# Optimization experiments

Measured on AMD Instinct MI355X. Metric: run time of the kernel, lower is better.

## Reference

```python
import jax, jax.numpy as jnp
import numpy as np

N = 256          # num_nodes per graph
B = 64           # batch_size (len(data.y))
NLAY = 3
F_IN = 5
NE = N * N       # num_edges per graph
NN = B * N       # total nodes
TEMP = 0.6
ALPHA = 0.1      # propagation residual alpha
BB_ALPHA = 0.8   # BBEdge_pred alpha
K = 2


def setup_inputs() -> dict:
    key = jax.random.key(0)
    ks = jax.random.split(key, 8)
    n_tril = N * (N + 1) // 2
    x = jax.random.normal(ks[0], (NN, F_IN), jnp.float32)
    # lower-triangular (incl. diagonal) entries of the learned adjacency
    edge_weight_param = jax.random.normal(ks[1], (n_tril,), jnp.float32)
    # BBEdge_pred params per layer (torch init: U(1.0,1.5), U(0.49,0.51))
    a_uc = 1.0 + 0.5 * jax.random.uniform(ks[2], (NLAY,), jnp.float32)
    b_uc = 0.49 + 0.02 * jax.random.uniform(ks[3], (NLAY,), jnp.float32)
    # randomness for Kumaraswamy pi sample and RelaxedBernoulli rsample
    u_pi = jax.random.uniform(ks[4], (NLAY,), jnp.float32)
    u_rb = jax.random.uniform(ks[5], (NLAY, NE), jnp.float32)
    lin_w = jax.random.normal(ks[6], (F_IN, 128), jnp.float32) / np.float32(np.sqrt(F_IN))
    lin_b = jnp.zeros((128,), jnp.float32)
    fc_w = jax.random.normal(ks[7], (128, 3), jnp.float32) / np.float32(np.sqrt(128))
    fc_b = jnp.zeros((3,), jnp.float32)
    # dense block-diagonal edge_index: graph b owns nodes [b*N, (b+1)*N); edge k=i*N+j -> (i,j)
    base = jnp.arange(N, dtype=jnp.int32)
    rows = jnp.repeat(base, N)
    cols = jnp.tile(base, N)
    offs = (jnp.arange(B, dtype=jnp.int32) * N)[:, None]
    edge_index = jnp.stack([(offs + rows[None, :]).reshape(-1),
                            (offs + cols[None, :]).reshape(-1)])
    batch = jnp.repeat(jnp.arange(B, dtype=jnp.int32), N)
    return {"x": x, "edge_weight_param": edge_weight_param, "a_uc": a_uc, "b_uc": b_uc,
            "u_pi": u_pi, "u_rb": u_rb, "lin_w": lin_w, "lin_b": lin_b,
            "fc_w": fc_w, "fc_b": fc_b, "edge_index": edge_index, "batch": batch}


def _forward(x, edge_weight_param, a_uc, b_uc, u_pi, u_rb,
             lin_w, lin_b, fc_w, fc_b, edge_index, batch):
    row, col = edge_index[0], edge_index[1]
    # symmetrized dense edge-weight matrix from tril params
    xs, ys = jnp.tril_indices(N)
    W = jnp.zeros((N, N), x.dtype).at[xs, ys].set(edge_weight_param)
    W = W + W.T - jnp.diag(jnp.diag(W))
    w_full = jnp.tile(W.reshape(-1), B)                      # [E]
    # GCN-style degree normalization (self-loops already on diagonal)
    deg = jax.ops.segment_sum(jnp.abs(w_full), row, num_segments=NN)
    dis = jnp.where(deg > 0, deg ** -0.5, 0.0)
    adj = dis[row] * w_full * dis[col]                       # [E]

    # Beta-Bernoulli edge keep-prob and RelaxedBernoulli masks
    a = jax.nn.softplus(jnp.clip(a_uc, -10.0, None))
    b = jax.nn.softplus(jnp.clip(b_uc, -10.0, 50.0))
    up = jnp.clip(u_pi, 1e-6, 1.0 - 1e-6)
    pi = (1.0 - up ** (1.0 / b)) ** (1.0 / a)                # [NLAY]
    ur = jnp.clip(u_rb, 1e-6, 1.0 - 1e-6)
    logits = jnp.log(pi) - jnp.log1p(-pi)                    # [NLAY]
    z = jax.nn.sigmoid((logits[:, None] + jnp.log(ur) - jnp.log1p(-ur)) / TEMP)  # [NLAY, NE]

    def conv(xx, w_e):
        # emb = alpha*x + (1-alpha)/K * scatter(col, w_e * x[row])
        msg = w_e[:, None] * xx[row]                          # [E, F]
        agg = jax.ops.segment_sum(msg, col, num_segments=NN)
        return ALPHA * xx + (1.0 - ALPHA) / K * agg

    emb = ALPHA * x
    # layer 0: masked adjacency
    x1 = conv(x, jnp.tile(z[0], B) * adj)
    emb = emb + (1.0 - ALPHA) * x1 / NLAY
    # layer 1 (middle): unmasked conv, then masked block conv (nblock=1, fp=5)
    x2 = conv(x1, adj)
    emb = emb + (1.0 - ALPHA) * x2 / NLAY
    x3 = jax.nn.relu(conv(x2[:, :F_IN], jnp.tile(z[1], B) * adj))  # dropout off (eval)
    # layer 2 (last)
    x4 = conv(x3, adj)
    emb = emb + (1.0 - ALPHA) * x4 / NLAY
    o = conv(x4, jnp.tile(z[2], B) * adj)
    out = jax.nn.relu(o @ lin_w + lin_b)                      # [NN, 128]

    # KL regularizer summed over layers
    euler = 0.577215664901532
    kld = ((1.0 - BB_ALPHA / a) * (-euler - jax.scipy.special.digamma(b) - 1.0 / b)
           + jnp.log(a * b + 1e-10) - jnp.log(jnp.float32(BB_ALPHA)) - (b - 1.0) / b)
    kld_loss = jnp.sum(kld)

    pooled = jax.ops.segment_sum(out, batch, num_segments=B)  # global_add_pool -> [B, 128]
    output = pooled @ fc_w + fc_b                             # [B, 3]
    drop_rates = pi[:, None]                                  # [NLAY, 1]
    return output, kld_loss, drop_rates


def reference(x, edge_weight_param, a_uc, b_uc, u_pi, u_rb,
              lin_w, lin_b, fc_w, fc_b, edge_index, batch):
    return _forward(x, edge_weight_param, a_uc, b_uc, u_pi, u_rb,
                    lin_w, lin_b, fc_w, fc_b, edge_index, batch)
```

## Files before the change

kernel.cpp:

```cpp
#include <hip/hip_runtime.h>
#include <math.h>

#define NN_ 256
#define BB_ 64
#define FF_ 5
#define NE_ 65536

#define OFF_SLA 0
#define OFF_SL1 65536
#define OFF_SL3 131072
#define OFF_SL5 196608
#define OFF_DIS 262144

__global__ __launch_bounds__(256) void build_all(
    const float* __restrict__ p, const float* __restrict__ u_rb,
    const float* __restrict__ a_uc, const float* __restrict__ b_uc,
    const float* __restrict__ u_pi, float* __restrict__ ws,
    float* __restrict__ out) {
  const int i = blockIdx.x, j = threadIdx.x;
  const int t = (i >= j) ? (i * (i + 1) / 2 + j) : (j * (j + 1) / 2 + i);
  const float w = p[t];

  __shared__ float sh[NN_];
  __shared__ float slg[3];
  __shared__ float skld[3];
  sh[j] = fabsf(w);

  if (j < 3) {
    const int l = j;
    const float au = fmaxf(a_uc[l], -10.0f);
    const float bu = fminf(fmaxf(b_uc[l], -10.0f), 50.0f);
    const float a = log1pf(expf(au));
    const float b = log1pf(expf(bu));
    const float up = fminf(fmaxf(u_pi[l], 1e-6f), 1.0f - 1e-6f);
    const float pi = powf(1.0f - powf(up, 1.0f / b), 1.0f / a);
    slg[l] = logf(pi) - log1pf(-pi);
    if (i == 0) {
      out[193 + l] = pi;
      float x = b, dg = 0.0f;
      while (x < 6.0f) { dg -= 1.0f / x; x += 1.0f; }
      const float inv = 1.0f / x, inv2 = inv * inv;
      dg += logf(x) - 0.5f * inv
            - inv2 * (1.0f / 12.0f - inv2 * (1.0f / 120.0f - inv2 * (1.0f / 252.0f)));
      const float euler = 0.577215664901532f;
      skld[l] = (1.0f - 0.8f / a) * (-euler - dg - 1.0f / b)
                + logf(a * b + 1e-10f) - logf(0.8f) - (b - 1.0f) / b;
    }
  }
  __syncthreads();

  for (int s = NN_ / 2; s > 0; s >>= 1) {
    if (j < s) sh[j] += sh[j + s];
    __syncthreads();
  }
  if (j == 0) {
    const float deg = sh[0];
    ws[OFF_DIS + i] = (deg > 0.0f) ? (1.0f / sqrtf(deg)) : 0.0f;
    if (i == 0) out[192] = skld[0] + skld[1] + skld[2];
  }

  const float lg0 = slg[0];
  const float lg1 = slg[1];
  const float lg2 = slg[2];
  const int idx = i * NN_ + j;
  const float inv_temp = 1.0f / 0.6f;

  ws[OFF_SLA + idx] = w;

  float u, v;
  u = fminf(fmaxf(u_rb[0 * NE_ + idx], 1e-6f), 1.0f - 1e-6f);
  v = (lg0 + logf(u) - log1pf(-u)) * inv_temp;
  ws[OFF_SL1 + idx] = w / (1.0f + expf(-v));

  u = fminf(fmaxf(u_rb[1 * NE_ + idx], 1e-6f), 1.0f - 1e-6f);
  v = (lg1 + logf(u) - log1pf(-u)) * inv_temp;
  ws[OFF_SL3 + idx] = w / (1.0f + expf(-v));

  u = fminf(fmaxf(u_rb[2 * NE_ + idx], 1e-6f), 1.0f - 1e-6f);
  v = (lg2 + logf(u) - log1pf(-u)) * inv_temp;
  ws[OFF_SL5 + idx] = w / (1.0f + expf(-v));
}

__global__ __launch_bounds__(1024) void batch_chain(
    const float* __restrict__ x0g, const float* __restrict__ ws,
    const float* __restrict__ lin_w, const float* __restrict__ lin_b,
    const float* __restrict__ fc_w, const float* __restrict__ fc_b,
    float* __restrict__ out) {
  const int b = blockIdx.x, tid = threadIdx.x;
  __shared__ float xbuf[2][NN_ * 8];
  __shared__ float sbuf[2][NN_ * 8];
  __shared__ float part[4 * NN_ * 8];
  __shared__ float sdis[NN_];
  float* Xc = xbuf[0];
  float* Xn = xbuf[1];
  float* Sc = sbuf[0];
  float* Sn = sbuf[1];

  for (int ii = tid; ii < NN_; ii += 1024) sdis[ii] = ws[OFF_DIS + ii];
  for (int idx = tid; idx < NN_ * FF_; idx += 1024) {
    const int i = idx / 5, f = idx - 5 * i;
    Xc[i * 8 + f] = x0g[b * (NN_ * FF_) + idx];
  }
  __syncthreads();
  for (int idx = tid; idx < 2048; idx += 1024)
    Sc[idx] = sdis[idx >> 3] * Xc[idx];
  __syncthreads();

  const int q = tid >> 8;
  const int j = tid & 255;
  const int k0 = q * 64;

#pragma unroll
  for (int l = 0; l < 5; ++l) {
    const float* __restrict__ Op =
        ws + (l == 0 ? OFF_SL1 : l == 2 ? OFF_SL3 : l == 4 ? OFF_SL5 : OFF_SLA)
        + j;
    float4 a03 = {0.f, 0.f, 0.f, 0.f};
    float a4 = 0.f;
#pragma unroll 8
    for (int k = k0; k < k0 + 64; ++k) {
      const float wv = Op[k * NN_];
      const float4 xv = *(const float4*)(Sc + k * 8);
      const float x4 = Sc[k * 8 + 4];
      a03.x += wv * xv.x; a03.y += wv * xv.y;
      a03.z += wv * xv.z; a03.w += wv * xv.w;
      a4 += wv * x4;
    }
    *(float4*)(part + tid * 8) = a03;
    part[tid * 8 + 4] = a4;
    __syncthreads();
    for (int idx = tid; idx < 2048; idx += 1024) {
      const float sum = part[idx] + part[2048 + idx] + part[4096 + idx] +
                        part[6144 + idx];
      const float dj = sdis[idx >> 3];
      float y = 0.1f * Xc[idx] + 0.45f * dj * sum;
      if (l == 2) y = fmaxf(y, 0.f);
      Xn[idx] = y;
      Sn[idx] = dj * y;
    }
    __syncthreads();
    float* tp = Xc; Xc = Xn; Xn = tp;
    tp = Sc; Sc = Sn; Sn = tp;
  }

  const int k = tid & 127, seg = tid >> 7;
  const float lw0 = lin_w[0 * 128 + k];
  const float lw1 = lin_w[1 * 128 + k];
  const float lw2 = lin_w[2 * 128 + k];
  const float lw3 = lin_w[3 * 128 + k];
  const float lw4 = lin_w[4 * 128 + k];
  const float lb = lin_b[k];
  float acc = 0.f;
  const int j0 = seg * 32;
#pragma unroll 4
  for (int jj = j0; jj < j0 + 32; ++jj) {
    const float4 ov = *(const float4*)(Xc + jj * 8);
    const float o4 = Xc[jj * 8 + 4];
    const float vv = lb + lw0 * ov.x + lw1 * ov.y + lw2 * ov.z +
                     lw3 * ov.w + lw4 * o4;
    acc += fmaxf(vv, 0.f);
  }
  part[seg * 128 + k] = acc;
  __syncthreads();
  if (tid < 128) {
    float s = 0.f;
#pragma unroll
    for (int s8 = 0; s8 < 8; ++s8) s += part[s8 * 128 + tid];
    part[tid] = s;
  }
  __syncthreads();
  if (tid < 3) {
    float s = fc_b[tid];
    for (int kk = 0; kk < 128; ++kk) s += part[kk] * fc_w[kk * 3 + tid];
    out[b * 3 + tid] = s;
  }
}

extern "C" void kernel_launch(void* const* d_in, const int* in_sizes, int n_in,
                              void* d_out, int out_size, void* d_ws,
                              size_t ws_size, hipStream_t stream) {
  const float* x      = (const float*)d_in[0];
  const float* p      = (const float*)d_in[1];
  const float* a_uc   = (const float*)d_in[2];
  const float* b_uc   = (const float*)d_in[3];
  const float* u_pi   = (const float*)d_in[4];
  const float* u_rb   = (const float*)d_in[5];
  const float* lin_w  = (const float*)d_in[6];
  const float* lin_b  = (const float*)d_in[7];
  const float* fc_w   = (const float*)d_in[8];
  const float* fc_b   = (const float*)d_in[9];
  float* out = (float*)d_out;
  float* ws  = (float*)d_ws;

  build_all<<<256, 256, 0, stream>>>(p, u_rb, a_uc, b_uc, u_pi, ws, out);
  batch_chain<<<64, 1024, 0, stream>>>(x, ws, lin_w, lin_b, fc_w, fc_b, out);
}
```

Measured before the change: 128.0 us.

## Split each graph's propagation chain across four blocks with global-memory barriers

The per-graph chain kernel moves from 64 blocks of 1024 threads to 256 blocks of 256 threads. Each of the four blocks per graph owns a quarter of the output rows. After every layer the blocks exchange the scaled features through global memory and meet at an atomic-counter barrier, and pooling is finished by one block per graph. This fills more compute units on the chip, but it adds inter-block spin-wait synchronisation, which assumes all blocks are co-resident, and extra global traffic.

New measurement: 161.7 us. +26.4%, slower.

```diff
diff --git a/kernel.cpp b/kernel.cpp
--- a/kernel.cpp
+++ b/kernel.cpp
@@ -11,6 +11,10 @@
 #define OFF_SL3 131072
 #define OFF_SL5 196608
 #define OFF_DIS 262144
+#define OFF_CNT 262400
+#define OFF_POOL 263168
+#define OFF_S0  327680
+#define OFF_S1  458752
 
 __global__ __launch_bounds__(256) void build_all(
     const float* __restrict__ p, const float* __restrict__ u_rb,
@@ -18,6 +22,13 @@
     const float* __restrict__ u_pi, float* __restrict__ ws,
     float* __restrict__ out) {
   const int i = blockIdx.x, j = threadIdx.x;
+
+  if (i == 0) {
+    int* cnt = (int*)(ws + OFF_CNT);
+    cnt[j] = 0;
+    cnt[256 + j] = 0;
+  }
+
   const int t = (i >= j) ? (i * (i + 1) / 2 + j) : (j * (j + 1) / 2 + i);
   const float w = p[t];
 
@@ -81,66 +92,82 @@
   ws[OFF_SL5 + idx] = w / (1.0f + expf(-v));
 }
 
-__global__ __launch_bounds__(1024) void batch_chain(
-    const float* __restrict__ x0g, const float* __restrict__ ws,
+__global__ __launch_bounds__(256) void chain_mb(
+    const float* __restrict__ x0g, float* __restrict__ ws,
     const float* __restrict__ lin_w, const float* __restrict__ lin_b,
     const float* __restrict__ fc_w, const float* __restrict__ fc_b,
     float* __restrict__ out) {
-  const int b = blockIdx.x, tid = threadIdx.x;
-  __shared__ float xbuf[2][NN_ * 8];
-  __shared__ float sbuf[2][NN_ * 8];
-  __shared__ float part[4 * NN_ * 8];
+  const int g = blockIdx.x >> 2;
+  const int q = blockIdx.x & 3;
+  const int tid = threadIdx.x;
+  const int j0 = tid & 63;
+  const int kq = tid >> 6;
+  const int j = q * 64 + j0;
+
+  __shared__ float S[NN_ * 8];
+  __shared__ float Xo[64 * 8];
+  __shared__ float part[4 * 64 * 8];
   __shared__ float sdis[NN_];
-  float* Xc = xbuf[0];
-  float* Xn = xbuf[1];
-  float* Sc = sbuf[0];
-  float* Sn = sbuf[1];
-
-  for (int ii = tid; ii < NN_; ii += 1024) sdis[ii] = ws[OFF_DIS + ii];
-  for (int idx = tid; idx < NN_ * FF_; idx += 1024) {
-    const int i = idx / 5, f = idx - 5 * i;
-    Xc[i * 8 + f] = x0g[b * (NN_ * FF_) + idx];
-  }
-  __syncthreads();
-  for (int idx = tid; idx < 2048; idx += 1024)
-    Sc[idx] = sdis[idx >> 3] * Xc[idx];
-  __syncthreads();
-
-  const int q = tid >> 8;
-  const int j = tid & 255;
-  const int k0 = q * 64;
+
+  int* const cnt = (int*)(ws + OFF_CNT) + g * 8;
+  float* const Sg0 = ws + OFF_S0 + g * 2048;
+  float* const Sg1 = ws + OFF_S1 + g * 2048;
+
+  for (int ii = tid; ii < NN_; ii += 256) sdis[ii] = ws[OFF_DIS + ii];
+  for (int idx = tid; idx < 2048; idx += 256) {
+    const int i = idx >> 3, f = idx & 7;
+    part[idx] = (f < 5) ? x0g[g * (NN_ * FF_) + i * 5 + f] : 0.0f;
+  }
+  __syncthreads();
+  for (int idx = tid; idx < 2048; idx += 256)
+    S[idx] = sdis[idx >> 3] * part[idx];
+  for (int idx = tid; idx < 512; idx += 256)
+    Xo[idx] = part[q * 512 + idx];
+  __syncthreads();
 
 #pragma unroll
   for (int l = 0; l < 5; ++l) {
     const float* __restrict__ Op =
         ws + (l == 0 ? OFF_SL1 : l == 2 ? OFF_SL3 : l == 4 ? OFF_SL5 : OFF_SLA)
         + j;
-    float4 a03 = {0.f, 0.f, 0.f, 0.f};
-    float a4 = 0.f;
+    float* const Sn = (l & 1) ? Sg1 : Sg0;
+    float a0 = 0.f, a1 = 0.f, a2 = 0.f, a3 = 0.f, a4 = 0.f;
+    const int kb = kq * 64;
 #pragma unroll 8
-    for (int k = k0; k < k0 + 64; ++k) {
+    for (int k = kb; k < kb + 64; ++k) {
       const float wv = Op[k * NN_];
-      const float4 xv = *(const float4*)(Sc + k * 8);
-      const float x4 = Sc[k * 8 + 4];
-      a03.x += wv * xv.x; a03.y += wv * xv.y;
-      a03.z += wv * xv.z; a03.w += wv * xv.w;
+      const float4 xv = *(const float4*)(S + k * 8);
+      const float x4 = S[k * 8 + 4];
+      a0 += wv * xv.x; a1 += wv * xv.y;
+      a2 += wv * xv.z; a3 += wv * xv.w;
       a4 += wv * x4;
     }
-    *(float4*)(part + tid * 8) = a03;
+    float4 t03 = {a0, a1, a2, a3};
+    *(float4*)(part + tid * 8) = t03;
     part[tid * 8 + 4] = a4;
     __syncthreads();
-    for (int idx = tid; idx < 2048; idx += 1024) {
-      const float sum = part[idx] + part[2048 + idx] + part[4096 + idx] +
-                        part[6144 + idx];
-      const float dj = sdis[idx >> 3];
-      float y = 0.1f * Xc[idx] + 0.45f * dj * sum;
+    for (int idx = tid; idx < 512; idx += 256) {
+      const float sum = part[idx] + part[512 + idx] + part[1024 + idx] +
+                        part[1536 + idx];
+      const float djj = sdis[q * 64 + (idx >> 3)];
+      float y = 0.1f * Xo[idx] + 0.45f * djj * sum;
       if (l == 2) y = fmaxf(y, 0.f);
-      Xn[idx] = y;
-      Sn[idx] = dj * y;
-    }
-    __syncthreads();
-    float* tp = Xc; Xc = Xn; Xn = tp;
-    tp = Sc; Sc = Sn; Sn = tp;
+      Xo[idx] = y;
+      if (l < 4) Sn[q * 512 + idx] = djj * y;
+    }
+    __syncthreads();
+    if (l < 4) {
+      if (tid == 0) {
+        __hip_atomic_fetch_add(&cnt[l], 1, __ATOMIC_ACQ_REL,
+                               __HIP_MEMORY_SCOPE_AGENT);
+        while (__hip_atomic_load(&cnt[l], __ATOMIC_ACQUIRE,
+                                 __HIP_MEMORY_SCOPE_AGENT) < 4)
+          __builtin_amdgcn_s_sleep(2);
+      }
+      __syncthreads();
+      for (int idx = tid; idx < 2048; idx += 256) S[idx] = Sn[idx];
+      __syncthreads();
+    }
   }
 
   const int k = tid & 127, seg = tid >> 7;
@@ -151,28 +178,41 @@
   const float lw4 = lin_w[4 * 128 + k];
   const float lb = lin_b[k];
   float acc = 0.f;
-  const int j0 = seg * 32;
+  const int r0 = seg * 32;
 #pragma unroll 4
-  for (int jj = j0; jj < j0 + 32; ++jj) {
-    const float4 ov = *(const float4*)(Xc + jj * 8);
-    const float o4 = Xc[jj * 8 + 4];
+  for (int r = r0; r < r0 + 32; ++r) {
+    const float4 ov = *(const float4*)(Xo + r * 8);
+    const float o4 = Xo[r * 8 + 4];
     const float vv = lb + lw0 * ov.x + lw1 * ov.y + lw2 * ov.z +
                      lw3 * ov.w + lw4 * o4;
     acc += fmaxf(vv, 0.f);
   }
   part[seg * 128 + k] = acc;
   __syncthreads();
-  if (tid < 128) {
-    float s = 0.f;
-#pragma unroll
-    for (int s8 = 0; s8 < 8; ++s8) s += part[s8 * 128 + tid];
-    part[tid] = s;
-  }
-  __syncthreads();
-  if (tid < 3) {
-    float s = fc_b[tid];
-    for (int kk = 0; kk < 128; ++kk) s += part[kk] * fc_w[kk * 3 + tid];
-    out[b * 3 + tid] = s;
+  if (tid < 128)
+    ws[OFF_POOL + (g * 4 + q) * 128 + tid] = part[tid] + part[128 + tid];
+  __syncthreads();
+  if (tid == 0)
+    __hip_atomic_fetch_add(&cnt[4], 1, __ATOMIC_ACQ_REL,
+                           __HIP_MEMORY_SCOPE_AGENT);
+
+  if (q == 0) {
+    if (tid == 0) {
+      while (__hip_atomic_load(&cnt[4], __ATOMIC_ACQUIRE,
+                               __HIP_MEMORY_SCOPE_AGENT) < 4)
+        __builtin_amdgcn_s_sleep(2);
+    }
+    __syncthreads();
+    if (tid < 128) {
+      const float* pp = ws + OFF_POOL + g * 512;
+      part[tid] = (pp[tid] + pp[128 + tid]) + pp[256 + tid] + pp[384 + tid];
+    }
+    __syncthreads();
+    if (tid < 3) {
+      float s = fc_b[tid];
+      for (int kk = 0; kk < 128; ++kk) s += part[kk] * fc_w[kk * 3 + tid];
+      out[g * 3 + tid] = s;
+    }
   }
 }
 
@@ -193,5 +233,5 @@
   float* ws  = (float*)d_ws;
 
   build_all<<<256, 256, 0, stream>>>(p, u_rb, a_uc, b_uc, u_pi, ws, out);
-  batch_chain<<<64, 1024, 0, stream>>>(x, ws, lin_w, lin_b, fc_w, fc_b, out);
+  chain_mb<<<256, 256, 0, stream>>>(x, ws, lin_w, lin_b, fc_w, fc_b, out);
 }
```
